# Kernel tuning notes

Hardware: AMD Instinct MI355X
Metric: run time of the kernel (lower is better)

Reference implementation:

```python
import jax, jax.numpy as jnp
import numpy as np

MARGIN = 0.01
MAX_PAIRS = 1000


def setup_inputs() -> dict:
    key = jax.random.key(0)
    k1, k2 = jax.random.split(key)
    n = 4096
    return {
        "predictions": jax.random.normal(k1, (n,), dtype=jnp.float32),
        "targets": jax.random.normal(k2, (n,), dtype=jnp.float32),
    }


def reference(predictions, targets):
    # Flatten as the torch module does for dim > 1 inputs.
    p = predictions.reshape(-1)
    t = targets.reshape(-1)
    n = p.shape[0]

    # Subsample indices exactly like the torch module (randperm -> first k),
    # using a fixed key so the baseline is deterministic.
    if n * (n - 1) // 2 > MAX_PAIRS:
        k = int(np.sqrt(MAX_PAIRS * 2))  # = 44
        idx = jax.random.permutation(jax.random.key(42), n)[:k]
    else:
        idx = jnp.arange(n)

    ps = p[idx]  # [k]
    ts = t[idx]  # [k]
    k = ps.shape[0]

    # Each unordered pair is visited exactly once in the original loop
    # (via the `i >= j: continue` on index values); the per-pair term is
    # symmetric under swapping, so a strict upper-triangle mask over
    # positions is equivalent.
    triu = jnp.triu(jnp.ones((k, k), dtype=bool), 1)  # [k,k]

    ta, tb = ts[:, None], ts[None, :]
    pa, pb = ps[:, None], ps[None, :]

    c1 = ta > tb + MARGIN  # target a ranks above b
    c2 = tb > ta + MARGIN  # target b ranks above a

    term = jnp.where(
        c1,
        jax.nn.relu(pb - pa + MARGIN),
        jnp.where(c2, jax.nn.relu(pa - pb + MARGIN), 0.0),
    )

    loss_sum = jnp.sum(jnp.where(triu, term, 0.0))
    count = jnp.sum(jnp.where(triu, c1 | c2, False).astype(jnp.float32))
    return jnp.where(count > 0, loss_sum / count, jnp.float32(0.0))
```

## Files before the change

kernel.cpp:

```cpp
#include <hip/hip_runtime.h>
#include <hip/hip_bf16.h>
#include <stdint.h>

namespace {

constexpr int N = 4096;
constexpr int K = 44;
constexpr float MARGIN = 0.01f;

struct U2 { uint32_t x, y; };

__host__ __device__ constexpr U2 tf(uint32_t k0, uint32_t k1, uint32_t x0, uint32_t x1) {
  const uint32_t ks0 = k0, ks1 = k1, ks2 = k0 ^ k1 ^ 0x1BD11BDAu;
  uint32_t ks[3] = {ks0, ks1, ks2};
  x0 += ks0; x1 += ks1;
  const int rot0[4] = {13, 15, 26, 6};
  const int rot1[4] = {17, 29, 16, 24};
  for (int i = 0; i < 5; ++i) {
    const int* r = (i & 1) ? rot1 : rot0;
    for (int j = 0; j < 4; ++j) {
      x0 += x1;
      x1 = (x1 << r[j]) | (x1 >> (32 - r[j]));
      x1 ^= x0;
    }
    x0 += ks[(i + 1) % 3];
    x1 += ks[(i + 2) % 3] + (uint32_t)(i + 1);
  }
  return {x0, x1};
}

constexpr U2 KEY1 = tf(0u, 42u, 0u, 0u);
constexpr U2 SUB1 = tf(0u, 42u, 0u, 1u);
constexpr U2 SUB2 = tf(KEY1.x, KEY1.y, 0u, 1u);

constexpr int JC = 8;
constexpr int JLEN = N / JC;

}

__global__ __launch_bounds__(256)
void RL_keys(uint64_t* __restrict__ keys1, uint64_t* __restrict__ keys2,
             uint32_t* __restrict__ rank1, uint32_t* __restrict__ rank2) {
  const uint32_t i = blockIdx.x * 256 + threadIdx.x;
  U2 a = tf(SUB1.x, SUB1.y, 0u, i);
  U2 b = tf(SUB2.x, SUB2.y, 0u, i);
  keys1[i] = ((uint64_t)(a.x ^ a.y) << 32) | i;
  keys2[i] = ((uint64_t)(b.x ^ b.y) << 32) | i;
  rank1[i] = 0u;
  rank2[i] = 0u;
}

__global__ __launch_bounds__(256)
void RL_rank(const uint64_t* __restrict__ keys1, const uint64_t* __restrict__ keys2,
             uint32_t* __restrict__ rank1, uint32_t* __restrict__ rank2) {
  __shared__ uint64_t kj[JLEN];
  const int b = blockIdx.x;
  const int pass = b >> 7;
  const int ic = b & 15;
  const int jc = (b >> 4) & 7;
  const uint64_t* __restrict__ keys = pass ? keys2 : keys1;
  uint32_t* __restrict__ rank = pass ? rank2 : rank1;
  const int tid = threadIdx.x;

  ((ulonglong2*)kj)[tid] = ((const ulonglong2*)(keys + jc * JLEN))[tid];
  __syncthreads();

  const int i = ic * 256 + tid;
  const uint64_t ki = keys[i];
  uint32_t cnt = 0;
#pragma unroll 8
  for (int j = 0; j < JLEN; ++j) cnt += (kj[j] < ki) ? 1u : 0u;
  atomicAdd(&rank[i], cnt);
}

__global__ __launch_bounds__(1024)
void RL_final(const uint32_t* __restrict__ rank1, const uint32_t* __restrict__ rank2,
              const float* __restrict__ pred, const float* __restrict__ targ,
              float* __restrict__ out) {
  __shared__ uint32_t inv1[N];
  __shared__ uint32_t selpos[K];
  __shared__ float sp[K], st[K];
  __shared__ float red_sum[16], red_cnt[16];
  const int tid = threadIdx.x;

  for (int i = tid; i < N; i += 1024) inv1[rank1[i]] = (uint32_t)i;
  for (int p = tid; p < N; p += 1024) {
    uint32_t r = rank2[p];
    if (r < K) selpos[r] = (uint32_t)p;
  }
  __syncthreads();

  if (tid < K) {
    uint32_t idx = inv1[selpos[tid]];
    sp[tid] = pred[idx];
    st[tid] = targ[idx];
  }
  __syncthreads();

  float lsum = 0.f, lcnt = 0.f;
  for (int q = tid; q < K * K; q += 1024) {
    int i = q / K, j = q % K;
    if (j > i) {
      float ta = st[i], tb = st[j], pa = sp[i], pb = sp[j];
      bool c1 = ta > tb + MARGIN;
      bool c2 = tb > ta + MARGIN;
      float term = c1 ? fmaxf(pb - pa + MARGIN, 0.f)
                      : (c2 ? fmaxf(pa - pb + MARGIN, 0.f) : 0.f);
      lsum += term;
      lcnt += (c1 || c2) ? 1.f : 0.f;
    }
  }
#pragma unroll
  for (int off = 32; off > 0; off >>= 1) {
    lsum += __shfl_down(lsum, off);
    lcnt += __shfl_down(lcnt, off);
  }
  const int wave = tid >> 6, lane = tid & 63;
  if (lane == 0) { red_sum[wave] = lsum; red_cnt[wave] = lcnt; }
  __syncthreads();
  if (tid == 0) {
    float s = 0.f, c = 0.f;
#pragma unroll
    for (int w = 0; w < 16; ++w) { s += red_sum[w]; c += red_cnt[w]; }
    out[0] = (c > 0.f) ? (s / c) : 0.f;
  }
}

extern "C" void kernel_launch(void* const* d_in, const int* in_sizes, int n_in,
                              void* d_out, int out_size, void* d_ws, size_t ws_size,
                              hipStream_t stream) {
  const float* pred = (const float*)d_in[0];
  const float* targ = (const float*)d_in[1];
  float* out = (float*)d_out;

  uint8_t* w = (uint8_t*)d_ws;
  uint64_t* keys1 = (uint64_t*)(w);
  uint64_t* keys2 = (uint64_t*)(w + 32 * 1024);
  uint32_t* rank1 = (uint32_t*)(w + 64 * 1024);
  uint32_t* rank2 = (uint32_t*)(w + 80 * 1024);

  hipLaunchKernelGGL(RL_keys, dim3(N / 256), dim3(256), 0, stream, keys1, keys2, rank1, rank2);
  hipLaunchKernelGGL(RL_rank, dim3(256), dim3(256), 0, stream, keys1, keys2, rank1, rank2);
  hipLaunchKernelGGL(RL_final, dim3(1), dim3(1024), 0, stream, rank1, rank2, pred, targ, out);
}
```

Before: 67.31 us.

## Fuse key generation into rank kernel and drop atomics and inverse permutation

Key generation moves into the rank kernel, so each 1024-thread block recomputes all 4096 keys for its pass into shared memory. This removes one launch and the global key buffers. Each block ranks 128 elements, with 32 lanes per group of 4 keys reduced by shuffles, so ranks are written directly without atomics or zero-initialisation. The final kernel composes the two permutations with a gather instead of building an inverse table in shared memory. The cost is redundant Threefry hashing in each of the 64 blocks.

```diff
diff --git a/kernel.cpp b/kernel.cpp
--- a/kernel.cpp
+++ b/kernel.cpp
@@ -33,65 +33,73 @@
 constexpr U2 SUB1 = tf(0u, 42u, 0u, 1u);
 constexpr U2 SUB2 = tf(KEY1.x, KEY1.y, 0u, 1u);
 
-constexpr int JC = 8;
-constexpr int JLEN = N / JC;
-
-}
-
-__global__ __launch_bounds__(256)
-void RL_keys(uint64_t* __restrict__ keys1, uint64_t* __restrict__ keys2,
-             uint32_t* __restrict__ rank1, uint32_t* __restrict__ rank2) {
-  const uint32_t i = blockIdx.x * 256 + threadIdx.x;
-  U2 a = tf(SUB1.x, SUB1.y, 0u, i);
-  U2 b = tf(SUB2.x, SUB2.y, 0u, i);
-  keys1[i] = ((uint64_t)(a.x ^ a.y) << 32) | i;
-  keys2[i] = ((uint64_t)(b.x ^ b.y) << 32) | i;
-  rank1[i] = 0u;
-  rank2[i] = 0u;
-}
-
-__global__ __launch_bounds__(256)
-void RL_rank(const uint64_t* __restrict__ keys1, const uint64_t* __restrict__ keys2,
-             uint32_t* __restrict__ rank1, uint32_t* __restrict__ rank2) {
-  __shared__ uint64_t kj[JLEN];
-  const int b = blockIdx.x;
-  const int pass = b >> 7;
-  const int ic = b & 15;
-  const int jc = (b >> 4) & 7;
-  const uint64_t* __restrict__ keys = pass ? keys2 : keys1;
-  uint32_t* __restrict__ rank = pass ? rank2 : rank1;
-  const int tid = threadIdx.x;
-
-  ((ulonglong2*)kj)[tid] = ((const ulonglong2*)(keys + jc * JLEN))[tid];
-  __syncthreads();
-
-  const int i = ic * 256 + tid;
-  const uint64_t ki = keys[i];
-  uint32_t cnt = 0;
-#pragma unroll 8
-  for (int j = 0; j < JLEN; ++j) cnt += (kj[j] < ki) ? 1u : 0u;
-  atomicAdd(&rank[i], cnt);
 }
 
 __global__ __launch_bounds__(1024)
-void RL_final(const uint32_t* __restrict__ rank1, const uint32_t* __restrict__ rank2,
+void RL_rank(uint32_t* __restrict__ rank) {
+  __shared__ uint64_t kj[N];
+  const int b = blockIdx.x;
+  const int pass = b >> 5;
+  const int ibase = (b & 31) * 128;
+  const int tid = threadIdx.x;
+  const U2 sub = pass ? SUB2 : SUB1;
+
+#pragma unroll
+  for (int q = 0; q < 4; ++q) {
+    const uint32_t j = (uint32_t)tid + q * 1024;
+    U2 r = tf(sub.x, sub.y, 0u, j);
+    kj[j] = ((uint64_t)(r.x ^ r.y) << 32) | j;
+  }
+  __syncthreads();
+
+  const int ig = tid >> 5;
+  const int jl = tid & 31;
+  const int i0 = ibase + ig * 4;
+  const uint64_t k0 = kj[i0], k1 = kj[i0 + 1], k2 = kj[i0 + 2], k3 = kj[i0 + 3];
+  uint32_t c0 = 0, c1 = 0, c2 = 0, c3 = 0;
+#pragma unroll 8
+  for (int s = 0; s < 128; ++s) {
+    const uint64_t v = kj[jl + 32 * s];
+    c0 += (v < k0) ? 1u : 0u;
+    c1 += (v < k1) ? 1u : 0u;
+    c2 += (v < k2) ? 1u : 0u;
+    c3 += (v < k3) ? 1u : 0u;
+  }
+#pragma unroll
+  for (int off = 16; off > 0; off >>= 1) {
+    c0 += __shfl_xor(c0, off);
+    c1 += __shfl_xor(c1, off);
+    c2 += __shfl_xor(c2, off);
+    c3 += __shfl_xor(c3, off);
+  }
+  if (jl == 0) {
+    rank[pass * N + i0]     = c0;
+    rank[pass * N + i0 + 1] = c1;
+    rank[pass * N + i0 + 2] = c2;
+    rank[pass * N + i0 + 3] = c3;
+  }
+}
+
+__global__ __launch_bounds__(1024)
+void RL_final(const uint32_t* __restrict__ rank,
               const float* __restrict__ pred, const float* __restrict__ targ,
               float* __restrict__ out) {
-  __shared__ uint32_t inv1[N];
-  __shared__ uint32_t selpos[K];
+  __shared__ uint32_t sel[K];
   __shared__ float sp[K], st[K];
   __shared__ float red_sum[16], red_cnt[16];
   const int tid = threadIdx.x;
 
-  for (int i = tid; i < N; i += 1024) inv1[rank1[i]] = (uint32_t)i;
-  for (int p = tid; p < N; p += 1024) {
-    uint32_t r = rank2[p];
-    if (r < K) selpos[r] = (uint32_t)p;
+#pragma unroll
+  for (int q = 0; q < 4; ++q) {
+    const int i = tid + q * 1024;
+    const uint32_t r1 = rank[i];
+    const uint32_t r2 = rank[N + r1];
+    if (r2 < K) sel[r2] = (uint32_t)i;
   }
   __syncthreads();
 
   if (tid < K) {
-    uint32_t idx = inv1[selpos[tid]];
+    const uint32_t idx = sel[tid];
     sp[tid] = pred[idx];
     st[tid] = targ[idx];
   }
@@ -132,14 +140,8 @@
   const float* pred = (const float*)d_in[0];
   const float* targ = (const float*)d_in[1];
   float* out = (float*)d_out;
+  uint32_t* rank = (uint32_t*)d_ws;
 
-  uint8_t* w = (uint8_t*)d_ws;
-  uint64_t* keys1 = (uint64_t*)(w);
-  uint64_t* keys2 = (uint64_t*)(w + 32 * 1024);
-  uint32_t* rank1 = (uint32_t*)(w + 64 * 1024);
-  uint32_t* rank2 = (uint32_t*)(w + 80 * 1024);
-
-  hipLaunchKernelGGL(RL_keys, dim3(N / 256), dim3(256), 0, stream, keys1, keys2, rank1, rank2);
-  hipLaunchKernelGGL(RL_rank, dim3(256), dim3(256), 0, stream, keys1, keys2, rank1, rank2);
-  hipLaunchKernelGGL(RL_final, dim3(1), dim3(1024), 0, stream, rank1, rank2, pred, targ, out);
+  hipLaunchKernelGGL(RL_rank, dim3(64), dim3(1024), 0, stream, rank);
+  hipLaunchKernelGGL(RL_final, dim3(1), dim3(1024), 0, stream, rank, pred, targ, out);
 }
```

Measured after the change: 68.76 us. +2.2%, slower.
